# Optimization experiments

Hardware: AMD Instinct MI355X
Metric: run time of the kernel (lower is better)

## Reference

```python
import jax, jax.numpy as jnp
import numpy as np

B, C_IN, C_OUT = 2, 32, 32
N_IN = 128 * 128            # input grid points
N_OUT = 128 * 128           # output grid points
KERNEL_SIZE = 9             # (3-1)*4 + 1 for kernel_shape=[3,4], piecewise_linear basis
NNZ = 1_500_000             # sparse entries in psi (kernel_size, n_out, n_in)


def setup_inputs() -> dict:
    key = jax.random.key(0)
    ks = jax.random.split(key, 8)
    scale = (1.0 / C_IN) ** 0.5  # sqrt(1/groupsize), groups=1
    return {
        "x": jax.random.normal(ks[0], (B, C_IN, N_IN), jnp.float32),
        "quadrature_weights": jax.random.uniform(ks[1], (N_IN,), jnp.float32, 0.5, 1.5) / N_IN,
        "psi_vals": jax.random.uniform(ks[2], (NNZ,), jnp.float32),
        "weight": scale * jax.random.normal(ks[3], (C_OUT, C_IN, KERNEL_SIZE), jnp.float32),
        "bias": jnp.zeros((C_OUT,), jnp.float32),
        "psi_idx_k": jax.random.randint(ks[4], (NNZ,), 0, KERNEL_SIZE, dtype=jnp.int32),
        "psi_idx_out": jax.random.randint(ks[5], (NNZ,), 0, N_OUT, dtype=jnp.int32),
        "psi_idx_in": jax.random.randint(ks[6], (NNZ,), 0, N_IN, dtype=jnp.int32),
        "n_out": N_OUT,
    }


def reference(x, quadrature_weights, psi_vals, weight, bias,
              psi_idx_k, psi_idx_out, psi_idx_in, n_out):
    # x: (B, C, n_in); weight: (O, C, K); psi is sparse (K, n_out, n_in)
    Bb, C, n_in = x.shape
    K = weight.shape[2]
    # pre-multiply by quadrature weights, layout (n_in, B, C) for gather
    xq = (x * quadrature_weights[None, None, :]).transpose(2, 0, 1)
    # gather-weight: contribution of each sparse entry  -> (nnz, B, C)
    contrib = xq[psi_idx_in] * psi_vals[:, None, None]
    # scatter-add into (kernel, out) bins == sparse psi @ xq
    seg = psi_idx_k * n_out + psi_idx_out
    xk = jax.ops.segment_sum(contrib, seg, num_segments=K * n_out)
    xk = xk.reshape(K, n_out, Bb, C)  # (K, n_out, B, C)
    # channel/kernel mixing with learned weight (groups=1)
    out = jnp.einsum("knbc,ock->bon", xk, weight) + bias[None, :, None]
    return out  # (B, out_channels, n_out)
```

## Files before the change

kernel.cpp:

```cpp
#include <hip/hip_runtime.h>

#define N_IN   16384
#define N_OUT  16384
#define KSZ    9
#define CIN    32
#define COUT   32
#define BC     64
#define NCB    256
#define CHA    4096
#define ECAP_A 8192
#define ROWS   144
#define XSTR   68
#define SCAP   2048

__global__ void k_xq(const float* __restrict__ x, const float* __restrict__ qw,
                     float* __restrict__ xq, const float* __restrict__ w,
                     float* __restrict__ wT, int* __restrict__ gcntA) {
    const int tid = threadIdx.x;
    if (blockIdx.x == 256) {
        for (int i = tid; i < COUT * CIN * KSZ; i += 256) {
            int o = i / (CIN * KSZ);
            int r = i - o * (CIN * KSZ);
            int c = r / KSZ;
            int k = r - c * KSZ;
            wT[((k * 8 + (o >> 2)) * 32 + c) * 4 + (o & 3)] = w[i];
        }
        if (tid < NCB) gcntA[tid] = 0;
        return;
    }
    __shared__ float tile[64 * 65];
    const int in0 = blockIdx.x * 64;
#pragma unroll
    for (int i = 0; i < 16; ++i) {
        int idx = tid + i * 256;
        int bcl = idx >> 6, inl = idx & 63;
        tile[bcl * 65 + inl] = x[bcl * N_IN + in0 + inl];
    }
    __syncthreads();
#pragma unroll
    for (int i = 0; i < 16; ++i) {
        int idx = tid + i * 256;
        int inl = idx >> 6, bcl = idx & 63;
        xq[(size_t)(in0 + inl) * BC + bcl] = tile[bcl * 65 + inl] * qw[in0 + inl];
    }
}

__global__ __launch_bounds__(512) void k_binA(const float* __restrict__ vals,
        const int* __restrict__ ik, const int* __restrict__ io, const int* __restrict__ ii,
        int* __restrict__ gcntA, float2* __restrict__ sivA, int nnz) {
    __shared__ int    cnt[NCB], cntE[NCB], gbase[NCB], cursor[NCB];
    __shared__ float2 slist[CHA];
    const int t = threadIdx.x, c = blockIdx.x;
    if (t < NCB) cnt[t] = 0;
    __syncthreads();
    const int base = c * CHA;
    const int e0   = base + t * 8;

    float vv[8]; int pk[8]; int bk[8]; bool hv[8];
    if (e0 + 8 <= nnz) {
        int4 a0 = *(const int4*)(io + e0),  a1 = *(const int4*)(io + e0 + 4);
        int4 b0 = *(const int4*)(ii + e0),  b1 = *(const int4*)(ii + e0 + 4);
        int4 k0 = *(const int4*)(ik + e0),  k1 = *(const int4*)(ik + e0 + 4);
        float4 d0 = *(const float4*)(vals + e0), d1 = *(const float4*)(vals + e0 + 4);
        int ov[8] = {a0.x, a0.y, a0.z, a0.w, a1.x, a1.y, a1.z, a1.w};
        int iv[8] = {b0.x, b0.y, b0.z, b0.w, b1.x, b1.y, b1.z, b1.w};
        int kv[8] = {k0.x, k0.y, k0.z, k0.w, k1.x, k1.y, k1.z, k1.w};
        float dv[8] = {d0.x, d0.y, d0.z, d0.w, d1.x, d1.y, d1.z, d1.w};
#pragma unroll
        for (int j = 0; j < 8; ++j) {
            hv[j] = true;
            bk[j] = ov[j] >> 6;
            pk[j] = (int)(((unsigned)(ov[j] >> 4) << 22)) | (iv[j] << 8) | (kv[j] * 16 + (ov[j] & 15));
            vv[j] = dv[j];
        }
    } else {
#pragma unroll
        for (int j = 0; j < 8; ++j) {
            int e = e0 + j;
            hv[j] = (e < nnz);
            if (hv[j]) {
                int o = io[e];
                bk[j] = o >> 6;
                pk[j] = (int)(((unsigned)(o >> 4) << 22)) | (ii[e] << 8) | (ik[e] * 16 + (o & 15));
                vv[j] = vals[e];
            } else { bk[j] = 0; pk[j] = 0; vv[j] = 0.f; }
        }
    }
#pragma unroll
    for (int j = 0; j < 8; ++j) if (hv[j]) atomicAdd(&cnt[bk[j]], 1);
    __syncthreads();
    if (t < NCB) {
        int cv = cnt[t];
        gbase[t] = t * ECAP_A + (cv ? atomicAdd(&gcntA[t], cv) : 0);
    }
    if (t < 64) {
        int carry = 0;
#pragma unroll
        for (int seg = 0; seg < 4; ++seg) {
            int idx = seg * 64 + t;
            int v = cnt[idx];
            int orig = v;
#pragma unroll
            for (int off = 1; off < 64; off <<= 1) {
                int u = __shfl_up(v, off);
                if (t >= off) v += u;
            }
            cntE[idx]   = carry + v - orig;
            cursor[idx] = carry + v - orig;
            carry += __shfl(v, 63);
        }
    }
    __syncthreads();
#pragma unroll
    for (int j = 0; j < 8; ++j) {
        if (hv[j]) {
            int pos = atomicAdd(&cursor[bk[j]], 1);
            slist[pos] = make_float2(vv[j], __int_as_float(pk[j]));
        }
    }
    __syncthreads();
    const int m = min(nnz - base, CHA);
    for (int p = t; p < m; p += 512) {
        float2 f = slist[p];
        int cb = (int)((unsigned)__float_as_int(f.y) >> 24);
        int dest = gbase[cb] + (p - cntE[cb]);
        if (dest < (cb + 1) * ECAP_A) sivA[dest] = f;
    }
}

__global__ __launch_bounds__(512) void k_fused6(const float* __restrict__ xq,
        const float2* __restrict__ sivA, const int* __restrict__ gcntA,
        const float* __restrict__ wT, const float* __restrict__ bias,
        float* __restrict__ out) {
    __shared__ __align__(16) float sxk[80 * XSTR];
    __shared__ float2 slist[SCAP];
    __shared__ int    rowStart[ROWS + 1];
    __shared__ int    cursor[ROWS];
    __shared__ int    mcur;
    const int tid  = threadIdx.x;
    const int lane = tid & 63;
    const int wv   = __builtin_amdgcn_readfirstlane(tid >> 6);
    const unsigned f = blockIdx.x;

    if (tid < ROWS) rowStart[tid] = 0;
    if (tid == 0) mcur = 0;
    __syncthreads();

    const int cb = (int)(f >> 2);
    const int mA = min(gcntA[cb], ECAP_A);
    const float2* src = sivA + (size_t)cb * ECAP_A;
    float2* tmp = (float2*)sxk;
    for (int i = tid; i < mA; i += 512) {
        float2 v = src[i];
        unsigned fid = (unsigned)__float_as_int(v.y) >> 22;
        if (fid == f) {
            int pos = atomicAdd(&mcur, 1);
            if (pos < SCAP) {
                tmp[pos] = v;
                atomicAdd(&rowStart[__float_as_int(v.y) & 0xFF], 1);
            }
        }
    }
    __syncthreads();
    const int m2 = min(mcur, SCAP);
    if (wv == 0) {
        int carry = 0;
#pragma unroll
        for (int i0 = 0; i0 < 192; i0 += 64) {
            int idx = i0 + lane;
            int v = (idx < ROWS) ? rowStart[idx] : 0;
            int orig = v;
#pragma unroll
            for (int off = 1; off < 64; off <<= 1) {
                int u = __shfl_up(v, off);
                if (lane >= off) v += u;
            }
            if (idx < ROWS) {
                int excl = carry + v - orig;
                rowStart[idx] = excl;
                cursor[idx]   = excl;
            }
            carry += __shfl(v, 63);
        }
        if (lane == 0) rowStart[ROWS] = carry;
    }
    __syncthreads();
    for (int i = tid; i < m2; i += 512) {
        float2 v = tmp[i];
        int pos = atomicAdd(&cursor[__float_as_int(v.y) & 0xFF], 1);
        slist[pos] = v;
    }
    __syncthreads();

    const char* xqb   = (const char*)xq;
    const int   lane4 = lane * 4;
    const int   h     = lane >> 4;
    const int   nl    = lane & 15;
    float acc[4] = {0.f, 0.f, 0.f, 0.f};

#pragma unroll
    for (int ph = 0; ph < 2; ++ph) {
        const int rbase = ph ? 80 : 0;
        const int rend  = ph ? 144 : 80;
        const int nrows = rend - rbase;
        for (int i = tid; i < nrows * XSTR; i += 512) sxk[i] = 0.f;
        __syncthreads();
        for (int r = rbase + wv; r < rend; r += 8) {
            const int a = rowStart[r], b = rowStart[r + 1];
            if (a >= b) continue;
            float acc0 = 0.f, acc1 = 0.f, acc2 = 0.f, acc3 = 0.f;
            int i = a;
            for (; i + 7 < b; i += 8) {
                float2 v0 = slist[i],     v1 = slist[i + 1], v2 = slist[i + 2], v3 = slist[i + 3];
                float2 v4 = slist[i + 4], v5 = slist[i + 5], v6 = slist[i + 6], v7 = slist[i + 7];
                acc0 += *(const float*)(xqb + ((__float_as_int(v0.y) & 0x3FFF00) + lane4)) * v0.x;
                acc1 += *(const float*)(xqb + ((__float_as_int(v1.y) & 0x3FFF00) + lane4)) * v1.x;
                acc2 += *(const float*)(xqb + ((__float_as_int(v2.y) & 0x3FFF00) + lane4)) * v2.x;
                acc3 += *(const float*)(xqb + ((__float_as_int(v3.y) & 0x3FFF00) + lane4)) * v3.x;
                acc0 += *(const float*)(xqb + ((__float_as_int(v4.y) & 0x3FFF00) + lane4)) * v4.x;
                acc1 += *(const float*)(xqb + ((__float_as_int(v5.y) & 0x3FFF00) + lane4)) * v5.x;
                acc2 += *(const float*)(xqb + ((__float_as_int(v6.y) & 0x3FFF00) + lane4)) * v6.x;
                acc3 += *(const float*)(xqb + ((__float_as_int(v7.y) & 0x3FFF00) + lane4)) * v7.x;
            }
            for (; i + 3 < b; i += 4) {
                float2 v0 = slist[i], v1 = slist[i + 1], v2 = slist[i + 2], v3 = slist[i + 3];
                acc0 += *(const float*)(xqb + ((__float_as_int(v0.y) & 0x3FFF00) + lane4)) * v0.x;
                acc1 += *(const float*)(xqb + ((__float_as_int(v1.y) & 0x3FFF00) + lane4)) * v1.x;
                acc2 += *(const float*)(xqb + ((__float_as_int(v2.y) & 0x3FFF00) + lane4)) * v2.x;
                acc3 += *(const float*)(xqb + ((__float_as_int(v3.y) & 0x3FFF00) + lane4)) * v3.x;
            }
            for (; i < b; ++i) {
                float2 v = slist[i];
                acc0 += *(const float*)(xqb + ((__float_as_int(v.y) & 0x3FFF00) + lane4)) * v.x;
            }
            sxk[(r - rbase) * XSTR + lane] = (acc0 + acc1) + (acc2 + acc3);
        }
        __syncthreads();
        if (lane < 32) {
            const int kbase = ph ? 5 : 0;
            const int kcnt  = ph ? 4 : 5;
            for (int kk = 0; kk < kcnt; ++kk) {
                const float* xr = &sxk[(kk * 16 + nl) * XSTR + h * 32];
                const float* wp = &wT[((kbase + kk) * 8 + wv) * 128];
#pragma unroll
                for (int c4 = 0; c4 < 8; ++c4) {
                    float4 xv = *(const float4*)&xr[c4 * 4];
#pragma unroll
                    for (int cc = 0; cc < 4; ++cc) {
                        float xval = (&xv.x)[cc];
#pragma unroll
                        for (int j = 0; j < 4; ++j)
                            acc[j] += xval * wp[(c4 * 4 + cc) * 4 + j];
                    }
                }
            }
        }
        __syncthreads();
    }

    if (lane < 32) {
        const int n0 = (int)f * 16;
#pragma unroll
        for (int j = 0; j < 4; ++j) {
            int o = wv * 4 + j;
            out[((size_t)h * COUT + o) * N_OUT + n0 + nl] = acc[j] + bias[o];
        }
    }
}

extern "C" void kernel_launch(void* const* d_in, const int* in_sizes, int n_in,
                              void* d_out, int out_size, void* d_ws, size_t ws_size,
                              hipStream_t stream) {
    const float* x    = (const float*)d_in[0];
    const float* qw   = (const float*)d_in[1];
    const float* vals = (const float*)d_in[2];
    const float* w    = (const float*)d_in[3];
    const float* bias = (const float*)d_in[4];
    const int*   ik   = (const int*)d_in[5];
    const int*   io   = (const int*)d_in[6];
    const int*   ii   = (const int*)d_in[7];
    const int    nnz  = in_sizes[2];
    const int    nchA = (nnz + CHA - 1) / CHA;

    char* ws = (char*)d_ws;
    float*  xq    = (float*)ws;  ws += (size_t)N_IN * BC * 4;
    float2* sivA  = (float2*)ws; ws += (size_t)NCB * ECAP_A * 8;
    int*    gcntA = (int*)ws;    ws += NCB * 4;
    float*  wT    = (float*)ws;  ws += (size_t)COUT * CIN * KSZ * 4;

    k_xq    <<<257, 256, 0, stream>>>(x, qw, xq, w, wT, gcntA);
    k_binA  <<<nchA, 512, 0, stream>>>(vals, ik, io, ii, gcntA, sivA, nnz);
    k_fused6<<<1024, 512, 0, stream>>>(xq, sivA, gcntA, wT, bias, (float*)d_out);
}
```

Baseline: 148.9 us.

## Scatter binned entries directly to global and re-read bucket in fused kernel

The binning kernel drops its shared-memory staging list and local prefix scan. Each entry now claims its global slot with a shared atomic cursor seeded from the global bucket offset, which gives uncoalesced direct writes but removes one barrier phase and 32KB of LDS. The fused kernel no longer compacts matching entries into a temporary buffer. It reads the bucket from global memory twice, once to count rows and once to place entries, trading extra L2 reads for less LDS traffic and fewer atomics. Clamps to SCAP are added for safety.

```diff
diff --git a/kernel.cpp b/kernel.cpp
--- a/kernel.cpp
+++ b/kernel.cpp
@@ -48,10 +48,9 @@
 __global__ __launch_bounds__(512) void k_binA(const float* __restrict__ vals,
         const int* __restrict__ ik, const int* __restrict__ io, const int* __restrict__ ii,
         int* __restrict__ gcntA, float2* __restrict__ sivA, int nnz) {
-    __shared__ int    cnt[NCB], cntE[NCB], gbase[NCB], cursor[NCB];
-    __shared__ float2 slist[CHA];
+    __shared__ int cur[NCB];
     const int t = threadIdx.x, c = blockIdx.x;
-    if (t < NCB) cnt[t] = 0;
+    if (t < NCB) cur[t] = 0;
     __syncthreads();
     const int base = c * CHA;
     const int e0   = base + t * 8;
@@ -87,48 +86,24 @@
         }
     }
 #pragma unroll
-    for (int j = 0; j < 8; ++j) if (hv[j]) atomicAdd(&cnt[bk[j]], 1);
+    for (int j = 0; j < 8; ++j) if (hv[j]) atomicAdd(&cur[bk[j]], 1);
     __syncthreads();
     if (t < NCB) {
-        int cv = cnt[t];
-        gbase[t] = t * ECAP_A + (cv ? atomicAdd(&gcntA[t], cv) : 0);
-    }
-    if (t < 64) {
-        int carry = 0;
-#pragma unroll
-        for (int seg = 0; seg < 4; ++seg) {
-            int idx = seg * 64 + t;
-            int v = cnt[idx];
-            int orig = v;
-#pragma unroll
-            for (int off = 1; off < 64; off <<= 1) {
-                int u = __shfl_up(v, off);
-                if (t >= off) v += u;
-            }
-            cntE[idx]   = carry + v - orig;
-            cursor[idx] = carry + v - orig;
-            carry += __shfl(v, 63);
-        }
+        int cv = cur[t];
+        cur[t] = t * ECAP_A + (cv ? atomicAdd(&gcntA[t], cv) : 0);
     }
     __syncthreads();
 #pragma unroll
     for (int j = 0; j < 8; ++j) {
         if (hv[j]) {
-            int pos = atomicAdd(&cursor[bk[j]], 1);
-            slist[pos] = make_float2(vv[j], __int_as_float(pk[j]));
-        }
-    }
-    __syncthreads();
-    const int m = min(nnz - base, CHA);
-    for (int p = t; p < m; p += 512) {
-        float2 f = slist[p];
-        int cb = (int)((unsigned)__float_as_int(f.y) >> 24);
-        int dest = gbase[cb] + (p - cntE[cb]);
-        if (dest < (cb + 1) * ECAP_A) sivA[dest] = f;
-    }
-}
-
-__global__ __launch_bounds__(512) void k_fused6(const float* __restrict__ xq,
+            int pos = atomicAdd(&cur[bk[j]], 1);
+            if (pos < (bk[j] + 1) * ECAP_A)
+                sivA[pos] = make_float2(vv[j], __int_as_float(pk[j]));
+        }
+    }
+}
+
+__global__ __launch_bounds__(512) void k_fused7(const float* __restrict__ xq,
         const float2* __restrict__ sivA, const int* __restrict__ gcntA,
         const float* __restrict__ wT, const float* __restrict__ bias,
         float* __restrict__ out) {
@@ -136,33 +111,22 @@
     __shared__ float2 slist[SCAP];
     __shared__ int    rowStart[ROWS + 1];
     __shared__ int    cursor[ROWS];
-    __shared__ int    mcur;
     const int tid  = threadIdx.x;
     const int lane = tid & 63;
     const int wv   = __builtin_amdgcn_readfirstlane(tid >> 6);
     const unsigned f = blockIdx.x;
 
     if (tid < ROWS) rowStart[tid] = 0;
-    if (tid == 0) mcur = 0;
     __syncthreads();
 
     const int cb = (int)(f >> 2);
     const int mA = min(gcntA[cb], ECAP_A);
     const float2* src = sivA + (size_t)cb * ECAP_A;
-    float2* tmp = (float2*)sxk;
     for (int i = tid; i < mA; i += 512) {
-        float2 v = src[i];
-        unsigned fid = (unsigned)__float_as_int(v.y) >> 22;
-        if (fid == f) {
-            int pos = atomicAdd(&mcur, 1);
-            if (pos < SCAP) {
-                tmp[pos] = v;
-                atomicAdd(&rowStart[__float_as_int(v.y) & 0xFF], 1);
-            }
-        }
-    }
-    __syncthreads();
-    const int m2 = min(mcur, SCAP);
+        int p = __float_as_int(src[i].y);
+        if (((unsigned)p >> 22) == f) atomicAdd(&rowStart[p & 0xFF], 1);
+    }
+    __syncthreads();
     if (wv == 0) {
         int carry = 0;
 #pragma unroll
@@ -185,10 +149,13 @@
         if (lane == 0) rowStart[ROWS] = carry;
     }
     __syncthreads();
-    for (int i = tid; i < m2; i += 512) {
-        float2 v = tmp[i];
-        int pos = atomicAdd(&cursor[__float_as_int(v.y) & 0xFF], 1);
-        slist[pos] = v;
+    for (int i = tid; i < mA; i += 512) {
+        float2 v = src[i];
+        int p = __float_as_int(v.y);
+        if (((unsigned)p >> 22) == f) {
+            int pos = atomicAdd(&cursor[p & 0xFF], 1);
+            if (pos < SCAP) slist[pos] = v;
+        }
     }
     __syncthreads();
 
@@ -206,7 +173,7 @@
         for (int i = tid; i < nrows * XSTR; i += 512) sxk[i] = 0.f;
         __syncthreads();
         for (int r = rbase + wv; r < rend; r += 8) {
-            const int a = rowStart[r], b = rowStart[r + 1];
+            const int a = min(rowStart[r], SCAP), b = min(rowStart[r + 1], SCAP);
             if (a >= b) continue;
             float acc0 = 0.f, acc1 = 0.f, acc2 = 0.f, acc3 = 0.f;
             int i = a;
@@ -290,5 +257,5 @@
 
     k_xq    <<<257, 256, 0, stream>>>(x, qw, xq, w, wT, gcntA);
     k_binA  <<<nchA, 512, 0, stream>>>(vals, ik, io, ii, gcntA, sivA, nnz);
-    k_fused6<<<1024, 512, 0, stream>>>(xq, sivA, gcntA, wT, bias, (float*)d_out);
-}
+    k_fused7<<<1024, 512, 0, stream>>>(xq, sivA, gcntA, wT, bias, (float*)d_out);
+}
```

Result: slower. 157.2 us (+5.6%).
